# Performance work log

Measured on AMD Instinct MI355X. Metric: run time of the kernel, lower is better.

Reference implementation:

```python
import jax, jax.numpy as jnp
import numpy as np

B, C, S, D = 4, 16, 512, 512
H = 8
HD = D // H
FFN = 2048
MAX_WL = 10000.0
ROPE_PCT = 0.5
EPS = 1e-5


def setup_inputs() -> dict:
    key = jax.random.key(0)
    ks = jax.random.split(key, 8)
    w = lambda k, shape: jax.random.normal(k, shape, jnp.float32) * 0.02
    return {
        "x": jax.random.normal(ks[0], (B, C, S, D), jnp.float32),
        "Wq": w(ks[1], (D, D)), "bq": jnp.zeros((D,), jnp.float32),
        "Wk": w(ks[2], (D, D)), "bk": jnp.zeros((D,), jnp.float32),
        "Wv": w(ks[3], (D, D)), "bv": jnp.zeros((D,), jnp.float32),
        "Wo": w(ks[4], (D, D)), "bo": jnp.zeros((D,), jnp.float32),
        "ln1_g": jnp.ones((D,), jnp.float32), "ln1_b": jnp.zeros((D,), jnp.float32),
        "ln3_g": jnp.ones((D,), jnp.float32), "ln3_b": jnp.zeros((D,), jnp.float32),
        "W1": w(ks[5], (D, FFN)), "b1": jnp.zeros((FFN,), jnp.float32),
        "W2": w(ks[6], (FFN, D)), "b2": jnp.zeros((D,), jnp.float32),
    }


def _layernorm(x, g, b):
    mu = jnp.mean(x, axis=-1, keepdims=True)
    var = jnp.mean((x - mu) ** 2, axis=-1, keepdims=True)
    return (x - mu) * jax.lax.rsqrt(var + EPS) * g + b


def _p_rope(x, pos):
    # partial rotary: rotate first ROPE_PCT fraction of rotation angles, pass rest through
    half = HD // 2
    rope_angles = int(ROPE_PCT * HD) // 2  # 16 for HD=64, pct=0.5
    exps = (2.0 / HD) * jnp.arange(rope_angles, dtype=jnp.float32)
    timescale = MAX_WL ** exps
    timescale = jnp.concatenate([timescale, jnp.full((half - rope_angles,), jnp.inf, jnp.float32)])
    ang = pos[:, None] / timescale[None, :]  # (S, half); inf timescale -> angle 0 -> identity
    sin, cos = jnp.sin(ang), jnp.cos(ang)
    x1, x2 = x[..., :half], x[..., half:]
    return jnp.concatenate([x1 * cos - x2 * sin, x2 * cos + x1 * sin], axis=-1)


def _forward(x, Wq, bq, Wk, bk, Wv, bv, Wo, bo, ln1_g, ln1_b, ln3_g, ln3_b, W1, b1, W2, b2):
    h = x.reshape(B * C, S, D)
    # --- temporal self-attention (pre-norm) ---
    hn = _layernorm(h, ln1_g, ln1_b)
    scaling = HD ** -0.5
    q = (hn @ Wq + bq) * scaling
    k = hn @ Wk + bk
    v = hn @ Wv + bv
    split = lambda t: t.reshape(B * C, S, H, HD).transpose(0, 2, 1, 3)  # (BC,H,S,HD)
    q, k, v = split(q), split(k), split(v)
    pos = jnp.arange(S, dtype=jnp.float32)
    q = _p_rope(q, pos)
    k = _p_rope(k, pos)
    attn = jax.nn.softmax(jnp.einsum('bhqd,bhkd->bhqk', q, k), axis=-1)
    o = jnp.einsum('bhqk,bhkd->bhqd', attn, v)
    o = o.transpose(0, 2, 1, 3).reshape(B * C, S, D) @ Wo + bo
    h = h + o
    # --- feed-forward (pre-norm) ---
    hn = _layernorm(h, ln3_g, ln3_b)
    ff = jax.nn.gelu(hn @ W1 + b1, approximate=False) @ W2 + b2
    h = h + ff
    return h.reshape(B, C, S, D)


def reference(x, Wq, bq, Wk, bk, Wv, bv, Wo, bo, ln1_g, ln1_b, ln3_g, ln3_b, W1, b1, W2, b2):
    return _forward(x, Wq, bq, Wk, bk, Wv, bv, Wo, bo, ln1_g, ln1_b, ln3_g, ln3_b, W1, b1, W2, b2)
```

## Files before the change

### kernel.cpp

```cpp
#include <hip/hip_runtime.h>
#include <math.h>

typedef unsigned short u16;
typedef __attribute__((ext_vector_type(8))) short bf16x8;
typedef __attribute__((ext_vector_type(4))) float f32x4;

#define MFMA16(a, b, c) __builtin_amdgcn_mfma_f32_16x16x32_bf16((a), (b), (c), 0, 0, 0)

__device__ __forceinline__ u16 f2bf(float f) {
    union { float f; unsigned u; } v; v.f = f;
    unsigned u = v.u;
    unsigned r = (u + 0x7FFFu + ((u >> 16) & 1u)) >> 16;
    return (u16)r;
}

__device__ __forceinline__ unsigned pack_bf16(float lo, float hi) {
    union { float f; unsigned u; } a, b; a.f = lo; b.f = hi;
    return __builtin_amdgcn_perm(b.u + 0x8000u, a.u + 0x8000u, 0x07060302u);
}

__device__ __forceinline__ float fexp2(float x) {
#if __has_builtin(__builtin_amdgcn_exp2f)
    return __builtin_amdgcn_exp2f(x);
#else
    return __expf(x * 0.6931471805599453f);
#endif
}

__device__ __forceinline__ void gl_lds16(const u16* g, u16* l) {
    __builtin_amdgcn_global_load_lds(
        (const __attribute__((address_space(1))) unsigned*)g,
        (__attribute__((address_space(3))) unsigned*)l, 16, 0, 0);
}

__global__ __launch_bounds__(256) void transpose_cvt_all(
    const float* __restrict__ Wq, const float* __restrict__ Wk,
    const float* __restrict__ Wv, const float* __restrict__ Wo,
    const float* __restrict__ W1, const float* __restrict__ W2,
    u16* __restrict__ wqt, u16* __restrict__ wkt, u16* __restrict__ wvt,
    u16* __restrict__ wot, u16* __restrict__ w1t, u16* __restrict__ w2t)
{
    __shared__ float tile[64][65];
    int fb = blockIdx.x;
    const float* src; u16* dst; int K, N, bx, by;
    if (fb < 256) {
        int w = fb >> 6, b = fb & 63;
        src = (w == 0) ? Wq : (w == 1) ? Wk : (w == 2) ? Wv : Wo;
        dst = (w == 0) ? wqt : (w == 1) ? wkt : (w == 2) ? wvt : wot;
        K = 512; N = 512; bx = b & 7; by = b >> 3;
    } else if (fb < 512) {
        int b = fb - 256; src = W1; dst = w1t; K = 512; N = 2048; bx = b & 31; by = b >> 5;
    } else {
        int b = fb - 512; src = W2; dst = w2t; K = 2048; N = 512; bx = b & 7; by = b >> 3;
    }
    int n0 = bx * 64, k0 = by * 64;
    int tx = threadIdx.x & 63, ty = threadIdx.x >> 6;
    #pragma unroll
    for (int i = ty; i < 64; i += 4)
        tile[i][tx] = src[(size_t)(k0 + i) * N + n0 + tx];
    __syncthreads();
    #pragma unroll
    for (int i = ty; i < 64; i += 4)
        dst[(size_t)(n0 + i) * K + k0 + tx] = f2bf(tile[tx][i]);
}

__global__ __launch_bounds__(256) void ln_kernel(const float* __restrict__ in,
                                                 u16* __restrict__ out,
                                                 const float* __restrict__ g,
                                                 const float* __restrict__ b) {
    int row = blockIdx.x;
    const float* rp = in + (size_t)row * 512;
    int t = threadIdx.x;
    float2 v = *(const float2*)(rp + t * 2);
    float s = v.x + v.y;
    float sq = v.x * v.x + v.y * v.y;
    #pragma unroll
    for (int off = 32; off > 0; off >>= 1) {
        s  += __shfl_down(s, off, 64);
        sq += __shfl_down(sq, off, 64);
    }
    __shared__ float red[8];
    __shared__ float stat[2];
    int wid = t >> 6;
    if ((t & 63) == 0) { red[wid] = s; red[wid + 4] = sq; }
    __syncthreads();
    if (t == 0) {
        float S = red[0] + red[1] + red[2] + red[3];
        float Q = red[4] + red[5] + red[6] + red[7];
        float mu = S * (1.0f / 512.0f);
        float var = Q * (1.0f / 512.0f) - mu * mu;
        stat[0] = mu;
        stat[1] = rsqrtf(var + 1e-5f);
    }
    __syncthreads();
    float mu = stat[0], inv = stat[1];
    int c = t * 2;
    float2 gv = *(const float2*)(g + c);
    float2 bv = *(const float2*)(b + c);
    ushort2 ov;
    ov.x = f2bf((v.x - mu) * inv * gv.x + bv.x);
    ov.y = f2bf((v.y - mu) * inv * gv.y + bv.y);
    *(ushort2*)(out + (size_t)row * 512 + c) = ov;
}

__global__ __launch_bounds__(256) void qkv_kernel(
    const u16* __restrict__ A,
    const u16* __restrict__ wqt, const u16* __restrict__ wkt, const u16* __restrict__ wvt,
    const float* __restrict__ bqp, const float* __restrict__ bkp, const float* __restrict__ bvp,
    u16* __restrict__ qb, u16* __restrict__ kb, u16* __restrict__ vb, float sclq)
{
    __shared__ u16 lA[2][128 * 32];
    __shared__ u16 lB[2][128 * 32];
    const int K = 512;
    int flat = blockIdx.y * gridDim.x + blockIdx.x;
    int xcd = flat & 7, slot = flat >> 3;
    int mt = xcd * 32 + slot / 12;
    int nt = slot % 12;
    int mode = nt >> 2;
    int m0 = mt * 128, n0 = (nt & 3) * 128;
    const u16* Bt = (mode == 0) ? wqt : (mode == 1) ? wkt : wvt;
    const float* bias = (mode == 0) ? bqp : (mode == 1) ? bkp : bvp;
    u16* outp = (mode == 0) ? qb : (mode == 1) ? kb : vb;

    int t = threadIdx.x;
    int wid = t >> 6, lane = t & 63, lm = lane & 15, lq = lane >> 4;
    int wm = (wid >> 1) * 64, wn = (wid & 1) * 64;
    const f32x4 zero = {0.f, 0.f, 0.f, 0.f};
    f32x4 acc[4][4];
    #pragma unroll
    for (int i = 0; i < 4; ++i)
        #pragma unroll
        for (int j = 0; j < 4; ++j) acc[i][j] = zero;

    int rr = t >> 2, cc = (t & 3) * 8;
    const u16* Ab = A + (size_t)(m0 + rr) * K + cc;
    const u16* Bb = Bt + (size_t)(n0 + rr) * K + cc;
    size_t pstep = (size_t)64 * K;
    int ldst = t * 8;

    for (int k0 = 0; k0 < K; k0 += 64) {
        #pragma unroll
        for (int h = 0; h < 2; ++h)
            #pragma unroll
            for (int p = 0; p < 2; ++p) {
                gl_lds16(Ab + k0 + h * 32 + p * pstep, lA[h] + p * 2048 + ldst);
                gl_lds16(Bb + k0 + h * 32 + p * pstep, lB[h] + p * 2048 + ldst);
            }
        __syncthreads();
        #pragma unroll
        for (int h = 0; h < 2; ++h) {
            bf16x8 af[4], bg[4];
            #pragma unroll
            for (int i = 0; i < 4; ++i) af[i] = *(const bf16x8*)&lA[h][(wm + i * 16 + lm) * 32 + lq * 8];
            #pragma unroll
            for (int i = 0; i < 4; ++i) bg[i] = *(const bf16x8*)&lB[h][(wn + i * 16 + lm) * 32 + lq * 8];
            #pragma unroll
            for (int i = 0; i < 4; ++i)
                #pragma unroll
                for (int j = 0; j < 4; ++j)
                    acc[i][j] = MFMA16(af[i], bg[j], acc[i][j]);
        }
        __syncthreads();
    }

    if (mode < 2) {
        float bv0 = bias[n0 + wn + 0 * 16 + lm];
        float bv1 = bias[n0 + wn + 1 * 16 + lm];
        float bv2 = bias[n0 + wn + 2 * 16 + lm];
        float bv3 = bias[n0 + wn + 3 * 16 + lm];
        float its = __expf((float)lm * -0.28782313662425572f);
        float scl = (mode == 0) ? sclq : 1.f;
        #pragma unroll
        for (int i = 0; i < 4; ++i) {
            #pragma unroll
            for (int r = 0; r < 4; ++r) {
                int gm = m0 + wm + i * 16 + lq * 4 + r;
                int s = gm & 511;
                float ang = (float)s * its;
                float sn = __sinf(ang), cs = __cosf(ang);
                float x1 = acc[i][0][r] + bv0;
                float x2 = acc[i][2][r] + bv2;
                float y0 = (x1 * cs - x2 * sn) * scl;
                float y2 = (x2 * cs + x1 * sn) * scl;
                float y1 = (acc[i][1][r] + bv1) * scl;
                float y3 = (acc[i][3][r] + bv3) * scl;
                size_t base = ((size_t)(gm >> 9)) * 262144 + (size_t)((n0 + wn) >> 6) * 32768
                            + (size_t)s * 64 + lm;
                outp[base +  0] = f2bf(y0);
                outp[base + 16] = f2bf(y1);
                outp[base + 32] = f2bf(y2);
                outp[base + 48] = f2bf(y3);
            }
        }
    } else {
        #pragma unroll
        for (int i = 0; i < 4; ++i) {
            #pragma unroll
            for (int j = 0; j < 4; ++j) {
                int gn = n0 + wn + j * 16 + lm;
                float bvv = bias[gn];
                #pragma unroll
                for (int r = 0; r < 4; ++r) {
                    int gm = m0 + wm + i * 16 + lq * 4 + r;
                    float v = acc[i][j][r] + bvv;
                    size_t idx = ((size_t)(gm >> 9)) * 262144 + (size_t)(gn >> 6) * 32768
                               + (size_t)(gn & 63) * 512 + (gm & 511);
                    outp[idx] = f2bf(v);
                }
            }
        }
    }
}

template<int MODE>
__global__ __launch_bounds__(256) void gemm_kernel(
    const u16* __restrict__ A, const u16* __restrict__ Bt,
    const float* __restrict__ bias, const float* __restrict__ res,
    void* __restrict__ outp, int M, int N, int K)
{
    __shared__ u16 lA[2][128 * 32];
    __shared__ u16 lB[2][128 * 32];
    int flat = blockIdx.y * gridDim.x + blockIdx.x;
    int xcd = flat & 7, slot = flat >> 3;
    int nb = gridDim.x;
    int mper = gridDim.y >> 3;
    int mt = xcd * mper + slot / nb;
    int nt = slot % nb;
    int m0 = mt * 128, n0 = nt * 128;

    int t = threadIdx.x;
    int wid = t >> 6, lane = t & 63, lm = lane & 15, lq = lane >> 4;
    int wm = (wid >> 1) * 64, wn = (wid & 1) * 64;
    const f32x4 zero = {0.f, 0.f, 0.f, 0.f};
    f32x4 acc[4][4];
    #pragma unroll
    for (int i = 0; i < 4; ++i)
        #pragma unroll
        for (int j = 0; j < 4; ++j) acc[i][j] = zero;

    int rr = t >> 2, cc = (t & 3) * 8;
    const u16* Ab = A + (size_t)(m0 + rr) * K + cc;
    const u16* Bb = Bt + (size_t)(n0 + rr) * K + cc;
    size_t pstep = (size_t)64 * K;
    int ldst = t * 8;

    for (int k0 = 0; k0 < K; k0 += 64) {
        #pragma unroll
        for (int h = 0; h < 2; ++h)
            #pragma unroll
            for (int p = 0; p < 2; ++p) {
                gl_lds16(Ab + k0 + h * 32 + p * pstep, lA[h] + p * 2048 + ldst);
                gl_lds16(Bb + k0 + h * 32 + p * pstep, lB[h] + p * 2048 + ldst);
            }
        __syncthreads();
        #pragma unroll
        for (int h = 0; h < 2; ++h) {
            bf16x8 af[4], bg[4];
            #pragma unroll
            for (int i = 0; i < 4; ++i) af[i] = *(const bf16x8*)&lA[h][(wm + i * 16 + lm) * 32 + lq * 8];
            #pragma unroll
            for (int i = 0; i < 4; ++i) bg[i] = *(const bf16x8*)&lB[h][(wn + i * 16 + lm) * 32 + lq * 8];
            #pragma unroll
            for (int i = 0; i < 4; ++i)
                #pragma unroll
                for (int j = 0; j < 4; ++j)
                    acc[i][j] = MFMA16(af[i], bg[j], acc[i][j]);
        }
        __syncthreads();
    }

    #pragma unroll
    for (int i = 0; i < 4; ++i) {
        #pragma unroll
        for (int j = 0; j < 4; ++j) {
            int gn = n0 + wn + j * 16 + lm;
            float bv = bias[gn];
            #pragma unroll
            for (int r = 0; r < 4; ++r) {
                int gm = m0 + wm + i * 16 + lq * 4 + r;
                float v = acc[i][j][r] + bv;
                if (MODE == 3) {
                    size_t idx = (size_t)gm * N + gn;
                    ((float*)outp)[idx] = v + res[idx];
                } else {
                    float gl = 0.5f * v * (1.f + erff(v * 0.70710678118654752f));
                    ((u16*)outp)[(size_t)gm * N + gn] = f2bf(gl);
                }
            }
        }
    }
}

__global__ __launch_bounds__(256) void attn_kernel(
    const u16* __restrict__ q, const u16* __restrict__ k,
    const u16* __restrict__ vt, u16* __restrict__ o)
{
    int flat = blockIdx.y * gridDim.x + blockIdx.x;
    int xcd = flat & 7, slot = flat >> 3;
    int nh = xcd * 64 + (slot >> 1);
    int qt = slot & 1;
    const u16* Qb = q + (size_t)nh * 32768 + (size_t)qt * 16384;
    const u16* Kb = k + (size_t)nh * 32768;
    const u16* Vb = vt + (size_t)nh * 32768;
    __shared__ u16 lK[64][72], lV[64][72];
    __shared__ u16 lP[4][16][72];
    int t = threadIdx.x, wid = t >> 6, lane = t & 63, lm = lane & 15, lq = lane >> 4;

    bf16x8 bq[4][2];
    #pragma unroll
    for (int sub = 0; sub < 4; ++sub) {
        const u16* qr = Qb + (size_t)(sub * 64 + wid * 16 + lm) * 64;
        bq[sub][0] = *(const bf16x8*)(qr + lq * 8);
        bq[sub][1] = *(const bf16x8*)(qr + 32 + lq * 8);
    }

    const f32x4 zero = {0.f, 0.f, 0.f, 0.f};
    f32x4 Oacc[4][4];
    float mo[4], l[4];
    #pragma unroll
    for (int s = 0; s < 4; ++s) {
        mo[s] = -INFINITY; l[s] = 0.f;
        #pragma unroll
        for (int d = 0; d < 4; ++d) Oacc[s][d] = zero;
    }

    for (int kt = 0; kt < 8; ++kt) {
        #pragma unroll
        for (int p = 0; p < 2; ++p) {
            int idx = p * 256 + t, row = idx >> 3, ch = (idx & 7) * 8;
            *(uint4*)&lK[row][ch] = *(const uint4*)(Kb + (size_t)(kt * 64 + row) * 64 + ch);
            *(uint4*)&lV[row][ch] = *(const uint4*)(Vb + (size_t)row * 512 + kt * 64 + ch);
        }
        __syncthreads();
        bf16x8 aK[4][2], aV[4][2];
        #pragma unroll
        for (int i = 0; i < 4; ++i) {
            aK[i][0] = *(const bf16x8*)&lK[i * 16 + lm][lq * 8];
            aK[i][1] = *(const bf16x8*)&lK[i * 16 + lm][32 + lq * 8];
            aV[i][0] = *(const bf16x8*)&lV[i * 16 + lm][lq * 8];
            aV[i][1] = *(const bf16x8*)&lV[i * 16 + lm][32 + lq * 8];
        }
        #pragma unroll
        for (int sub = 0; sub < 4; ++sub) {
            f32x4 sc[4];
            #pragma unroll
            for (int i = 0; i < 4; ++i) {
                f32x4 z = MFMA16(aK[i][0], bq[sub][0], zero);
                sc[i] = MFMA16(aK[i][1], bq[sub][1], z);
            }
            float mx = sc[0][0];
            #pragma unroll
            for (int i = 0; i < 4; ++i)
                #pragma unroll
                for (int r = 0; r < 4; ++r) mx = fmaxf(mx, sc[i][r]);
            mx = fmaxf(mx, __shfl_xor(mx, 16, 64));
            mx = fmaxf(mx, __shfl_xor(mx, 32, 64));
            float mn = fmaxf(mo[sub], mx);
            float al = fexp2(mo[sub] - mn);
            float pv[4][4], sum = 0.f;
            #pragma unroll
            for (int i = 0; i < 4; ++i)
                #pragma unroll
                for (int r = 0; r < 4; ++r) { pv[i][r] = fexp2(sc[i][r] - mn); sum += pv[i][r]; }
            sum += __shfl_xor(sum, 16, 64);
            sum += __shfl_xor(sum, 32, 64);
            l[sub] = l[sub] * al + sum;
            mo[sub] = mn;
            #pragma unroll
            for (int dn = 0; dn < 4; ++dn) Oacc[sub][dn] *= al;
            #pragma unroll
            for (int i = 0; i < 4; ++i) {
                uint2 w2;
                w2.x = pack_bf16(pv[i][0], pv[i][1]);
                w2.y = pack_bf16(pv[i][2], pv[i][3]);
                *(uint2*)&lP[wid][lm][i * 16 + lq * 4] = w2;
            }
            bf16x8 bp0 = *(const bf16x8*)&lP[wid][lm][lq * 8];
            bf16x8 bp1 = *(const bf16x8*)&lP[wid][lm][32 + lq * 8];
            #pragma unroll
            for (int dn = 0; dn < 4; ++dn) {
                Oacc[sub][dn] = MFMA16(aV[dn][0], bp0, Oacc[sub][dn]);
                Oacc[sub][dn] = MFMA16(aV[dn][1], bp1, Oacc[sub][dn]);
            }
        }
        __syncthreads();
    }
    int bc = nh >> 3, h = nh & 7;
    #pragma unroll
    for (int sub = 0; sub < 4; ++sub) {
        float inv = 1.f / l[sub];
        size_t orow = ((size_t)(bc * 512 + qt * 256 + sub * 64 + wid * 16 + lm)) * 512 + h * 64;
        #pragma unroll
        for (int dn = 0; dn < 4; ++dn) {
            uint2 w2;
            w2.x = pack_bf16(Oacc[sub][dn][0] * inv, Oacc[sub][dn][1] * inv);
            w2.y = pack_bf16(Oacc[sub][dn][2] * inv, Oacc[sub][dn][3] * inv);
            *(uint2*)(o + orow + dn * 16 + lq * 4) = w2;
        }
    }
}

extern "C" void kernel_launch(void* const* d_in, const int* in_sizes, int n_in,
                              void* d_out, int out_size, void* d_ws, size_t ws_size,
                              hipStream_t stream) {
    const float* x    = (const float*)d_in[0];
    const float* Wq   = (const float*)d_in[1];
    const float* bq   = (const float*)d_in[2];
    const float* Wk   = (const float*)d_in[3];
    const float* bk   = (const float*)d_in[4];
    const float* Wv   = (const float*)d_in[5];
    const float* bv   = (const float*)d_in[6];
    const float* Wo   = (const float*)d_in[7];
    const float* bo   = (const float*)d_in[8];
    const float* ln1g = (const float*)d_in[9];
    const float* ln1b = (const float*)d_in[10];
    const float* ln3g = (const float*)d_in[11];
    const float* ln3b = (const float*)d_in[12];
    const float* W1   = (const float*)d_in[13];
    const float* b1   = (const float*)d_in[14];
    const float* W2   = (const float*)d_in[15];
    const float* b2   = (const float*)d_in[16];

    char* ws = (char*)d_ws;
    u16*  hn  = (u16*)(ws + 0ull);
    u16*  qb  = (u16*)(ws + 33554432ull);
    u16*  kb  = (u16*)(ws + 67108864ull);
    u16*  vb  = (u16*)(ws + 100663296ull);
    u16*  ob  = (u16*)(ws + 134217728ull);
    u16*  ffa = (u16*)(ws + 33554432ull);
    float* h1 = (float*)(ws + 167772160ull);
    u16*  wqt = (u16*)(ws + 234881024ull);
    u16*  wkt = (u16*)(ws + 235405312ull);
    u16*  wvt = (u16*)(ws + 235929600ull);
    u16*  wot = (u16*)(ws + 236453888ull);
    u16*  w1t = (u16*)(ws + 236978176ull);
    u16*  w2t = (u16*)(ws + 239075328ull);

    dim3 blk(256);
    transpose_cvt_all<<<768, blk, 0, stream>>>(Wq, Wk, Wv, Wo, W1, W2,
                                               wqt, wkt, wvt, wot, w1t, w2t);

    ln_kernel<<<32768, blk, 0, stream>>>(x, hn, ln1g, ln1b);

    qkv_kernel<<<dim3(12, 256), blk, 0, stream>>>(hn, wqt, wkt, wvt, bq, bk, bv,
                                                  qb, kb, vb, 0.125f * 1.4426950408889634f);

    attn_kernel<<<dim3(2, 512), blk, 0, stream>>>(qb, kb, vb, ob);

    gemm_kernel<3><<<dim3(4, 256), blk, 0, stream>>>(ob, wot, bo, x, h1, 32768, 512, 512);

    ln_kernel<<<32768, blk, 0, stream>>>(h1, hn, ln3g, ln3b);

    gemm_kernel<4><<<dim3(16, 256), blk, 0, stream>>>(hn, w1t, b1, nullptr, ffa, 32768, 2048, 512);
    gemm_kernel<3><<<dim3(4, 256), blk, 0, stream>>>(ffa, w2t, b2, h1, (float*)d_out, 32768, 512, 2048);
}
```

Measured before the change: 636.4 us.

## Replace 128x128 GEMMs with 256x256 tiles, swizzled LDS and deeper pipelined prefetch

All dense GEMMs (QKV, output projection, FFN1, FFN2) now use a shared 256x256 tile core with 512 threads, 128 KB of XOR-swizzled LDS, and a staged prefetch schedule. Each quarter of the next k-step's tiles is loaded between MFMA groups, with vmcnt waits, barriers and s_setprio raising MFMA priority. The aim is more operand reuse per LDS byte, fewer bank conflicts, and loads overlapped with compute. In exchange, occupancy drops to one large workgroup per CU, register pressure rises from 128 accumulator floats per thread, and the grids shrink to 256 blocks for the N=512 GEMMs, which may leave CUs underused.

New measurement: 600.2 us. -5.7%, faster.

```diff
diff --git a/kernel.cpp b/kernel.cpp
--- a/kernel.cpp
+++ b/kernel.cpp
@@ -103,78 +103,166 @@
     *(ushort2*)(out + (size_t)row * 512 + c) = ov;
 }
 
-__global__ __launch_bounds__(256) void qkv_kernel(
+
+#define BAR()   __builtin_amdgcn_s_barrier()
+#define LGKM0() asm volatile("s_waitcnt lgkmcnt(0)" ::: "memory")
+#define VM6()   asm volatile("s_waitcnt vmcnt(6)" ::: "memory")
+#define PRIO1() __builtin_amdgcn_s_setprio(1)
+#define PRIO0() __builtin_amdgcn_s_setprio(0)
+
+__device__ __forceinline__ bf16x8 ldfrag(const u16* __restrict__ base, int R, int ko, int lq) {
+    int o = (ko + lq * 8) ^ ((R & 7) * 8);
+    return *(const bf16x8*)(base + R * 64 + o);
+}
+
+__device__ __forceinline__ void stage_half(const u16* __restrict__ g, int ldk,
+                                           u16* __restrict__ dst, int t) {
+    #pragma unroll
+    for (int p = 0; p < 2; ++p) {
+        int idx = p * 512 + t;
+        int row = idx >> 3;
+        int col = ((idx & 7) * 8) ^ ((row & 7) * 8);
+        gl_lds16(g + (size_t)row * ldk + col, dst + idx * 8);
+    }
+}
+
+__device__ __forceinline__ void gemm256_core(
+    const u16* __restrict__ A, const u16* __restrict__ Bt, int K,
+    int m0, int n0, int t, u16* __restrict__ smem, f32x4 (&acc)[8][4])
+{
+    const int NS = K >> 6;
+    const int wid = t >> 6, lane = t & 63;
+    const int lm = lane & 15, lq = lane >> 4;
+    const int wm_ = wid >> 2;
+    const int wn_ = wid & 3;
+    const int wbh = wn_ >> 1;
+    const int wbr = (wn_ & 1) * 64;
+
+    auto reg = [&](int buf, int ab, int half) -> u16* {
+        return smem + (((buf << 1) | ab) * 2 + half) * 8192;
+    };
+    auto stage = [&](int h) {
+        int u = h >> 2;
+        if (u >= NS) return;
+        int w = h & 3;
+        int k0 = u << 6, buf = u & 1;
+        if (w < 2)
+            stage_half(Bt + (size_t)(n0 + w * 128) * K + k0, K, reg(buf, 1, w), t);
+        else
+            stage_half(A + (size_t)(m0 + (w - 2) * 128) * K + k0, K, reg(buf, 0, w - 2), t);
+    };
+
+    #pragma unroll
+    for (int i = 0; i < 8; ++i)
+        #pragma unroll
+        for (int j = 0; j < 4; ++j) acc[i][j] = (f32x4){0.f, 0.f, 0.f, 0.f};
+
+    #pragma unroll
+    for (int h = 0; h < 7; ++h) stage(h);
+    VM6();
+    BAR();
+
+    for (int s = 0; s < NS; ++s) {
+        const u16* As = reg(s & 1, 0, wm_);
+        const u16* Bs = reg(s & 1, 1, wbh);
+        bf16x8 aF[4][2], bF[4][2];
+        #pragma unroll
+        for (int i = 0; i < 4; ++i) {
+            aF[i][0] = ldfrag(As, i * 16 + lm, 0, lq);
+            aF[i][1] = ldfrag(As, i * 16 + lm, 32, lq);
+        }
+        #pragma unroll
+        for (int j = 0; j < 4; ++j) {
+            bF[j][0] = ldfrag(Bs, wbr + j * 16 + lm, 0, lq);
+            bF[j][1] = ldfrag(Bs, wbr + j * 16 + lm, 32, lq);
+        }
+        stage(4 * (s + 1) + 3);
+        BAR(); LGKM0(); PRIO1();
+        #pragma unroll
+        for (int i = 0; i < 4; ++i)
+            #pragma unroll
+            for (int j = 0; j < 2; ++j) {
+                acc[i][j] = MFMA16(aF[i][0], bF[j][0], acc[i][j]);
+                acc[i][j] = MFMA16(aF[i][1], bF[j][1], acc[i][j]);
+            }
+        PRIO0(); BAR();
+        stage(4 * (s + 2) + 0);
+        BAR(); LGKM0(); PRIO1();
+        #pragma unroll
+        for (int i = 0; i < 4; ++i)
+            #pragma unroll
+            for (int j = 0; j < 2; ++j) {
+                acc[i][2 + j] = MFMA16(aF[i][0], bF[2 + j][0], acc[i][2 + j]);
+                acc[i][2 + j] = MFMA16(aF[i][1], bF[2 + j][1], acc[i][2 + j]);
+            }
+        PRIO0(); BAR();
+        #pragma unroll
+        for (int i = 0; i < 4; ++i) {
+            aF[i][0] = ldfrag(As, 64 + i * 16 + lm, 0, lq);
+            aF[i][1] = ldfrag(As, 64 + i * 16 + lm, 32, lq);
+        }
+        stage(4 * (s + 2) + 1);
+        BAR(); LGKM0(); PRIO1();
+        #pragma unroll
+        for (int i = 0; i < 4; ++i)
+            #pragma unroll
+            for (int j = 0; j < 2; ++j) {
+                acc[4 + i][j] = MFMA16(aF[i][0], bF[j][0], acc[4 + i][j]);
+                acc[4 + i][j] = MFMA16(aF[i][1], bF[j][1], acc[4 + i][j]);
+            }
+        PRIO0(); BAR();
+        stage(4 * (s + 2) + 2);
+        BAR(); LGKM0(); PRIO1();
+        #pragma unroll
+        for (int i = 0; i < 4; ++i)
+            #pragma unroll
+            for (int j = 0; j < 2; ++j) {
+                acc[4 + i][2 + j] = MFMA16(aF[i][0], bF[2 + j][0], acc[4 + i][2 + j]);
+                acc[4 + i][2 + j] = MFMA16(aF[i][1], bF[2 + j][1], acc[4 + i][2 + j]);
+            }
+        PRIO0();
+        VM6();
+        BAR();
+    }
+}
+
+__global__ __launch_bounds__(512) void qkv256_kernel(
     const u16* __restrict__ A,
     const u16* __restrict__ wqt, const u16* __restrict__ wkt, const u16* __restrict__ wvt,
     const float* __restrict__ bqp, const float* __restrict__ bkp, const float* __restrict__ bvp,
     u16* __restrict__ qb, u16* __restrict__ kb, u16* __restrict__ vb, float sclq)
 {
-    __shared__ u16 lA[2][128 * 32];
-    __shared__ u16 lB[2][128 * 32];
-    const int K = 512;
-    int flat = blockIdx.y * gridDim.x + blockIdx.x;
+    __shared__ u16 smem[65536];
+    int flat = blockIdx.x;
     int xcd = flat & 7, slot = flat >> 3;
-    int mt = xcd * 32 + slot / 12;
-    int nt = slot % 12;
-    int mode = nt >> 2;
-    int m0 = mt * 128, n0 = (nt & 3) * 128;
+    int g = xcd * 96 + slot;
+    int mt = g / 6, nt = g % 6;
+    int mode = nt >> 1;
+    int m0 = mt * 256, nb0 = (nt & 1) * 256;
     const u16* Bt = (mode == 0) ? wqt : (mode == 1) ? wkt : wvt;
     const float* bias = (mode == 0) ? bqp : (mode == 1) ? bkp : bvp;
     u16* outp = (mode == 0) ? qb : (mode == 1) ? kb : vb;
 
     int t = threadIdx.x;
+    f32x4 acc[8][4];
+    gemm256_core(A, Bt, 512, m0, nb0, t, smem, acc);
+
     int wid = t >> 6, lane = t & 63, lm = lane & 15, lq = lane >> 4;
-    int wm = (wid >> 1) * 64, wn = (wid & 1) * 64;
-    const f32x4 zero = {0.f, 0.f, 0.f, 0.f};
-    f32x4 acc[4][4];
-    #pragma unroll
-    for (int i = 0; i < 4; ++i)
-        #pragma unroll
-        for (int j = 0; j < 4; ++j) acc[i][j] = zero;
-
-    int rr = t >> 2, cc = (t & 3) * 8;
-    const u16* Ab = A + (size_t)(m0 + rr) * K + cc;
-    const u16* Bb = Bt + (size_t)(n0 + rr) * K + cc;
-    size_t pstep = (size_t)64 * K;
-    int ldst = t * 8;
-
-    for (int k0 = 0; k0 < K; k0 += 64) {
-        #pragma unroll
-        for (int h = 0; h < 2; ++h)
-            #pragma unroll
-            for (int p = 0; p < 2; ++p) {
-                gl_lds16(Ab + k0 + h * 32 + p * pstep, lA[h] + p * 2048 + ldst);
-                gl_lds16(Bb + k0 + h * 32 + p * pstep, lB[h] + p * 2048 + ldst);
-            }
-        __syncthreads();
-        #pragma unroll
-        for (int h = 0; h < 2; ++h) {
-            bf16x8 af[4], bg[4];
-            #pragma unroll
-            for (int i = 0; i < 4; ++i) af[i] = *(const bf16x8*)&lA[h][(wm + i * 16 + lm) * 32 + lq * 8];
-            #pragma unroll
-            for (int i = 0; i < 4; ++i) bg[i] = *(const bf16x8*)&lB[h][(wn + i * 16 + lm) * 32 + lq * 8];
-            #pragma unroll
-            for (int i = 0; i < 4; ++i)
-                #pragma unroll
-                for (int j = 0; j < 4; ++j)
-                    acc[i][j] = MFMA16(af[i], bg[j], acc[i][j]);
-        }
-        __syncthreads();
-    }
+    int rowb = m0 + (wid >> 2) * 128;
+    int colb = nb0 + (wid & 3) * 64;
 
     if (mode < 2) {
-        float bv0 = bias[n0 + wn + 0 * 16 + lm];
-        float bv1 = bias[n0 + wn + 1 * 16 + lm];
-        float bv2 = bias[n0 + wn + 2 * 16 + lm];
-        float bv3 = bias[n0 + wn + 3 * 16 + lm];
+        float bv0 = bias[colb + 0 * 16 + lm];
+        float bv1 = bias[colb + 1 * 16 + lm];
+        float bv2 = bias[colb + 2 * 16 + lm];
+        float bv3 = bias[colb + 3 * 16 + lm];
         float its = __expf((float)lm * -0.28782313662425572f);
         float scl = (mode == 0) ? sclq : 1.f;
         #pragma unroll
-        for (int i = 0; i < 4; ++i) {
+        for (int i = 0; i < 8; ++i) {
             #pragma unroll
             for (int r = 0; r < 4; ++r) {
-                int gm = m0 + wm + i * 16 + lq * 4 + r;
+                int gm = rowb + i * 16 + lq * 4 + r;
                 int s = gm & 511;
                 float ang = (float)s * its;
                 float sn = __sinf(ang), cs = __cosf(ang);
@@ -184,7 +272,7 @@
                 float y2 = (x2 * cs + x1 * sn) * scl;
                 float y1 = (acc[i][1][r] + bv1) * scl;
                 float y3 = (acc[i][3][r] + bv3) * scl;
-                size_t base = ((size_t)(gm >> 9)) * 262144 + (size_t)((n0 + wn) >> 6) * 32768
+                size_t base = ((size_t)(gm >> 9)) * 262144 + (size_t)(colb >> 6) * 32768
                             + (size_t)s * 64 + lm;
                 outp[base +  0] = f2bf(y0);
                 outp[base + 16] = f2bf(y1);
@@ -194,90 +282,53 @@
         }
     } else {
         #pragma unroll
-        for (int i = 0; i < 4; ++i) {
+        for (int i = 0; i < 8; ++i)
             #pragma unroll
             for (int j = 0; j < 4; ++j) {
-                int gn = n0 + wn + j * 16 + lm;
+                int gn = colb + j * 16 + lm;
                 float bvv = bias[gn];
                 #pragma unroll
                 for (int r = 0; r < 4; ++r) {
-                    int gm = m0 + wm + i * 16 + lq * 4 + r;
+                    int gm = rowb + i * 16 + lq * 4 + r;
                     float v = acc[i][j][r] + bvv;
                     size_t idx = ((size_t)(gm >> 9)) * 262144 + (size_t)(gn >> 6) * 32768
                                + (size_t)(gn & 63) * 512 + (gm & 511);
                     outp[idx] = f2bf(v);
                 }
             }
-        }
     }
 }
 
 template<int MODE>
-__global__ __launch_bounds__(256) void gemm_kernel(
+__global__ __launch_bounds__(512) void gemm256_kernel(
     const u16* __restrict__ A, const u16* __restrict__ Bt,
     const float* __restrict__ bias, const float* __restrict__ res,
     void* __restrict__ outp, int M, int N, int K)
 {
-    __shared__ u16 lA[2][128 * 32];
-    __shared__ u16 lB[2][128 * 32];
-    int flat = blockIdx.y * gridDim.x + blockIdx.x;
+    __shared__ u16 smem[65536];
+    int flat = blockIdx.x;
+    int nbt = N >> 8;
+    int nwg = (M >> 8) * nbt;
     int xcd = flat & 7, slot = flat >> 3;
-    int nb = gridDim.x;
-    int mper = gridDim.y >> 3;
-    int mt = xcd * mper + slot / nb;
-    int nt = slot % nb;
-    int m0 = mt * 128, n0 = nt * 128;
+    int g = xcd * (nwg >> 3) + slot;
+    int mt = g / nbt, nt = g % nbt;
+    int m0 = mt * 256, n0 = nt * 256;
 
     int t = threadIdx.x;
+    f32x4 acc[8][4];
+    gemm256_core(A, Bt, K, m0, n0, t, smem, acc);
+
     int wid = t >> 6, lane = t & 63, lm = lane & 15, lq = lane >> 4;
-    int wm = (wid >> 1) * 64, wn = (wid & 1) * 64;
-    const f32x4 zero = {0.f, 0.f, 0.f, 0.f};
-    f32x4 acc[4][4];
-    #pragma unroll
-    for (int i = 0; i < 4; ++i)
-        #pragma unroll
-        for (int j = 0; j < 4; ++j) acc[i][j] = zero;
-
-    int rr = t >> 2, cc = (t & 3) * 8;
-    const u16* Ab = A + (size_t)(m0 + rr) * K + cc;
-    const u16* Bb = Bt + (size_t)(n0 + rr) * K + cc;
-    size_t pstep = (size_t)64 * K;
-    int ldst = t * 8;
-
-    for (int k0 = 0; k0 < K; k0 += 64) {
-        #pragma unroll
-        for (int h = 0; h < 2; ++h)
-            #pragma unroll
-            for (int p = 0; p < 2; ++p) {
-                gl_lds16(Ab + k0 + h * 32 + p * pstep, lA[h] + p * 2048 + ldst);
-                gl_lds16(Bb + k0 + h * 32 + p * pstep, lB[h] + p * 2048 + ldst);
-            }
-        __syncthreads();
-        #pragma unroll
-        for (int h = 0; h < 2; ++h) {
-            bf16x8 af[4], bg[4];
-            #pragma unroll
-            for (int i = 0; i < 4; ++i) af[i] = *(const bf16x8*)&lA[h][(wm + i * 16 + lm) * 32 + lq * 8];
-            #pragma unroll
-            for (int i = 0; i < 4; ++i) bg[i] = *(const bf16x8*)&lB[h][(wn + i * 16 + lm) * 32 + lq * 8];
-            #pragma unroll
-            for (int i = 0; i < 4; ++i)
-                #pragma unroll
-                for (int j = 0; j < 4; ++j)
-                    acc[i][j] = MFMA16(af[i], bg[j], acc[i][j]);
-        }
-        __syncthreads();
-    }
-
-    #pragma unroll
-    for (int i = 0; i < 4; ++i) {
+    int rowb = m0 + (wid >> 2) * 128, colb = n0 + (wid & 3) * 64;
+    #pragma unroll
+    for (int i = 0; i < 8; ++i)
         #pragma unroll
         for (int j = 0; j < 4; ++j) {
-            int gn = n0 + wn + j * 16 + lm;
+            int gn = colb + j * 16 + lm;
             float bv = bias[gn];
             #pragma unroll
             for (int r = 0; r < 4; ++r) {
-                int gm = m0 + wm + i * 16 + lq * 4 + r;
+                int gm = rowb + i * 16 + lq * 4 + r;
                 float v = acc[i][j][r] + bv;
                 if (MODE == 3) {
                     size_t idx = (size_t)gm * N + gn;
@@ -288,7 +339,6 @@
                 }
             }
         }
-    }
 }
 
 __global__ __launch_bounds__(256) void attn_kernel(
@@ -442,15 +492,19 @@
 
     ln_kernel<<<32768, blk, 0, stream>>>(x, hn, ln1g, ln1b);
 
-    qkv_kernel<<<dim3(12, 256), blk, 0, stream>>>(hn, wqt, wkt, wvt, bq, bk, bv,
-                                                  qb, kb, vb, 0.125f * 1.4426950408889634f);
+    qkv256_kernel<<<768, dim3(512), 0, stream>>>(hn, wqt, wkt, wvt, bq, bk, bv,
+                                                 qb, kb, vb,
+                                                 0.125f * 1.4426950408889634f);
 
     attn_kernel<<<dim3(2, 512), blk, 0, stream>>>(qb, kb, vb, ob);
 
-    gemm_kernel<3><<<dim3(4, 256), blk, 0, stream>>>(ob, wot, bo, x, h1, 32768, 512, 512);
+    gemm256_kernel<3><<<256, dim3(512), 0, stream>>>(ob, wot, bo, x, h1,
+                                                     32768, 512, 512);
 
     ln_kernel<<<32768, blk, 0, stream>>>(h1, hn, ln3g, ln3b);
 
-    gemm_kernel<4><<<dim3(16, 256), blk, 0, stream>>>(hn, w1t, b1, nullptr, ffa, 32768, 2048, 512);
-    gemm_kernel<3><<<dim3(4, 256), blk, 0, stream>>>(ffa, w2t, b2, h1, (float*)d_out, 32768, 512, 2048);
-}
+    gemm256_kernel<4><<<1024, dim3(512), 0, stream>>>(hn, w1t, b1, nullptr, ffa,
+                                                      32768, 2048, 512);
+    gemm256_kernel<3><<<256, dim3(512), 0, stream>>>(ffa, w2t, b2, h1,
+                                                     (float*)d_out, 32768, 512, 2048);
+}
```
